# Kernel optimization log

Hardware: AMD Instinct MI355X
Metric: run time of the kernel (lower is better)

## Reference

```python
import jax, jax.numpy as jnp
import numpy as np

SWITCH_W = 30.0
TOL = 5
DECAY = 0.7
FP_PEN = 10.0
INV_PEN = 100.0
CLASS_W = jnp.array([1.0, 1.0, SWITCH_W, SWITCH_W], dtype=jnp.float32)


def setup_inputs() -> dict:
    key = jax.random.key(0)
    k1, k2, k3 = jax.random.split(key, 3)
    B, S, C = 512, 8192, 4
    logits = jax.random.normal(k1, (B, S, C), dtype=jnp.float32)
    labels = jax.random.randint(k2, (B, S), 0, 4, dtype=jnp.int32)
    # sprinkle ignore_index (-100) positions like real padded sequences
    drop = jax.random.uniform(k3, (B, S)) < 0.05
    labels = jnp.where(drop, jnp.int32(-100), labels)
    return {"logits": logits, "labels": labels}


def _mode_multiplier(labels, preds):
    """Sequential state machine over time; carry = (pred_mode, true_mode) per batch row."""
    B, S = labels.shape

    def step(carry, xs):
        pm, tm = carry
        lab, pred = xs  # [B] each
        valid = lab != -100
        # invalid transition penalty on predicted switches
        bad = ((pred == 2) & (pm == 0)) | ((pred == 3) & (pm == 1))
        pen = jnp.where(valid & bad, INV_PEN, 1.0)
        new_pm = jnp.where(valid, jnp.where((pred == 0) | (pred == 2), 0, 1), pm)
        # reward correct mode switches (true label agrees with pred switch)
        good = ((lab == 2) & (tm == 1) & (pred == 2)) | ((lab == 3) & (tm == 0) & (pred == 3))
        bonus = jnp.where(valid & good, 0.1, 1.0)
        new_tm = jnp.where(valid & ((lab == 0) | (lab == 2)), 0,
                           jnp.where(valid & ((lab == 1) | (lab == 3)), 1, tm))
        return (new_pm, new_tm), pen * bonus

    init = (jnp.zeros((B,), jnp.int32), jnp.zeros((B,), jnp.int32))
    _, mult = jax.lax.scan(step, init, (labels.T, preds.T))
    return mult.T  # [B, S]


def _nearest_dist(mask):
    """For each position, distance to nearest True in the same row; BIG if none."""
    B, S = mask.shape
    BIG = jnp.int32(S + TOL + 2)

    def f(c, m):
        c = jnp.where(m, jnp.int32(0), jnp.minimum(c + 1, BIG))
        return c, c

    init = jnp.full((B,), BIG, jnp.int32)
    _, fwd = jax.lax.scan(f, init, mask.T)
    _, bwd = jax.lax.scan(f, init, mask[:, ::-1].T)
    return jnp.minimum(fwd.T, bwd.T[:, ::-1])


def _loss(logits, labels):
    preds = jnp.argmax(logits, axis=-1).astype(jnp.int32)
    valid = labels != -100
    labs = jnp.where(valid, labels, 0)
    logp = jax.nn.log_softmax(logits, axis=-1)
    ce = -jnp.take_along_axis(logp, labs[..., None], axis=-1)[..., 0] * CLASS_W[labs]

    mult = _mode_multiplier(labels, preds)
    for c in (2, 3):
        true_m = labels == c
        pred_m = preds == c
        d_true = _nearest_dist(true_m)
        d_pred = _nearest_dist(pred_m)
        has_true = true_m.any(axis=1, keepdims=True)
        has_pred = pred_m.any(axis=1, keepdims=True)
        # multipliers at predicted-switch positions
        mp = jnp.where(
            pred_m,
            jnp.where(
                has_true,
                jnp.where(d_true == 0, 0.1,
                          jnp.where(d_true <= TOL, DECAY ** d_true.astype(jnp.float32), FP_PEN)),
                FP_PEN * 2.0),
            1.0)
        # multipliers at true-switch positions
        mt = jnp.where(
            true_m,
            jnp.where(has_pred, jnp.where(d_pred > TOL, 2.0, 1.0), 3.0),
            1.0)
        mult = mult * mp * mt

    vf = valid.astype(ce.dtype)
    total = (ce * mult * vf).sum()
    return total / jnp.maximum(vf.sum(), 1.0)


def reference(logits, labels):
    return _loss(logits, labels)
```

## Files before the change

kernel.cpp:

```cpp
#include <hip/hip_runtime.h>
#include <math.h>

#define BROWS 512
#define SLEN  8192
#define NT    1024
#define CHUNK (SLEN / NT)
#define NWRD  (SLEN / 32)
#define MWRD  (NWRD + 2)
#define CEPAD (SLEN + SLEN/8)

__device__ __forceinline__ int win_dist(const unsigned int* __restrict__ M, int t) {
    int sI = t + 27;
    int w  = sI >> 5;
    int off = sI & 31;
    unsigned long long val =
        ((unsigned long long)M[w] | ((unsigned long long)M[w + 1] << 32)) >> off;
    unsigned int win = (unsigned int)val & 0x7FFu;
    if (win & 32u) return 0;
    unsigned int dn = win & 31u;
    unsigned int up = (win >> 6) & 31u;
    int d = 99;
    if (dn) d = 5 - (31 - __clz((int)dn));
    if (up) { int du = __ffs((int)up); if (du < d) d = du; }
    return d;
}

__device__ __forceinline__ float decay_pow(int d) {
    return (d == 1) ? 0.7f : (d == 2) ? 0.49f : (d == 3) ? 0.343f
         : (d == 4) ? 0.2401f : 0.16807f;
}

__global__ __launch_bounds__(NT, 8) void row_loss_kernel(
    const float* __restrict__ logits, const int* __restrict__ labels,
    double* __restrict__ psum, unsigned int* __restrict__ pcnt)
{
    __shared__ float         s_ce[CEPAD];
    __shared__ unsigned char s_pk[SLEN];
    __shared__ unsigned int  s_m[4][MWRD];
    __shared__ unsigned int  s_wave[16];
    __shared__ unsigned int  s_wavex[16];
    __shared__ unsigned int  s_flags;
    __shared__ double        s_red[16];
    __shared__ int           s_redc[16];

    const int row  = blockIdx.x;
    const int tid  = threadIdx.x;
    const int lane = tid & 63;
    const int wid  = tid >> 6;

    for (int i = tid; i < 4 * MWRD; i += NT) ((unsigned int*)s_m)[i] = 0u;
    if (tid == 0) s_flags = 0u;

    const float4* lg4 = (const float4*)(logits + (size_t)row * SLEN * 4);
    const int*    lb  = labels + (size_t)row * SLEN;

    #pragma unroll
    for (int k = 0; k < CHUNK; ++k) {
        int t = k * NT + tid;
        float4 v = lg4[t];
        int lab = lb[t];
        int pred = 0; float best = v.x;
        if (v.y > best) { best = v.y; pred = 1; }
        if (v.z > best) { best = v.z; pred = 2; }
        if (v.w > best) { best = v.w; pred = 3; }
        bool valid = (lab != -100);
        int l = valid ? (lab & 3) : 0;
        float se = __expf(v.x - best) + __expf(v.y - best) +
                   __expf(v.z - best) + __expf(v.w - best);
        float lse = best + __logf(se);
        float xl = (l == 0) ? v.x : (l == 1) ? v.y : (l == 2) ? v.z : v.w;
        float wc = (l >= 2) ? 30.0f : 1.0f;
        s_ce[t + (t >> 3)] = valid ? (lse - xl) * wc : 0.0f;
        s_pk[t] = (unsigned char)(pred | (l << 2) | (valid ? 16 : 0));
    }
    __syncthreads();

    const int base = tid * CHUNK;
    unsigned int mt2 = 0, mp2 = 0, mt3 = 0, mp3 = 0;
    unsigned int summary = 0;
    #pragma unroll
    for (int i = 0; i < CHUNK; ++i) {
        unsigned int pk = s_pk[base + i];
        int pred = pk & 3, l = (pk >> 2) & 3;
        bool valid = (pk & 16) != 0;
        if (pred == 2) mp2 |= 1u << i;
        if (pred == 3) mp3 |= 1u << i;
        if (valid && l == 2) mt2 |= 1u << i;
        if (valid && l == 3) mt3 |= 1u << i;
        if (valid) summary = 4u | (unsigned)(pred & 1) | ((unsigned)(l & 1) << 1);
    }
    {
        int wi = 1 + (tid >> 2);
        int sh = (tid & 3) * 8;
        if (mt2) atomicOr(&s_m[0][wi], mt2 << sh);
        if (mp2) atomicOr(&s_m[1][wi], mp2 << sh);
        if (mt3) atomicOr(&s_m[2][wi], mt3 << sh);
        if (mp3) atomicOr(&s_m[3][wi], mp3 << sh);
    }
    {
        unsigned int fl = (mt2 ? 1u : 0u) | (mp2 ? 2u : 0u) |
                          (mt3 ? 4u : 0u) | (mp3 ? 8u : 0u);
        #pragma unroll
        for (int s = 32; s > 0; s >>= 1) fl |= __shfl_xor(fl, s);
        if (lane == 0 && fl) atomicOr(&s_flags, fl);
    }

    unsigned int inc = summary;
    #pragma unroll
    for (int st = 1; st < 64; st <<= 1) {
        unsigned int o = __shfl_up(inc, st);
        if (lane >= st && !(inc & 4u)) inc = o;
    }
    unsigned int exc = __shfl_up(inc, 1);
    if (lane == 0) exc = 0u;
    if (lane == 63) s_wave[wid] = inc;
    __syncthreads();
    if (wid == 0) {
        unsigned int wv = (lane < 16) ? s_wave[lane] : 0u;
        #pragma unroll
        for (int st = 1; st < 16; st <<= 1) {
            unsigned int o = __shfl_up(wv, st);
            if (lane >= st && !(wv & 4u)) wv = o;
        }
        unsigned int wex = __shfl_up(wv, 1);
        if (lane == 0) wex = 0u;
        if (lane < 16) s_wavex[lane] = wex;
    }
    __syncthreads();

    unsigned int pre = (exc & 4u) ? exc : s_wavex[wid];
    int pm = (int)(pre & 1u), tm = (int)((pre >> 1) & 1u);
    unsigned int flags = s_flags;
    const bool hasT2 = flags & 1u, hasP2 = flags & 2u;
    const bool hasT3 = flags & 4u, hasP3 = flags & 8u;

    float acc = 0.0f;
    int cnt = 0;
    #pragma unroll
    for (int i = 0; i < CHUNK; ++i) {
        int t = base + i;
        unsigned int pk = s_pk[t];
        int pred = pk & 3, l = (pk >> 2) & 3;
        bool valid = (pk & 16) != 0;
        float m = 1.0f;
        if (valid) {
            bool bad = (pred == 2 && pm == 0) || (pred == 3 && pm == 1);
            if (bad) m *= 100.0f;
            bool good = (l == 2 && tm == 1 && pred == 2) ||
                        (l == 3 && tm == 0 && pred == 3);
            if (good) m *= 0.1f;
            pm = pred & 1;
            tm = l & 1;
            cnt++;
        }
        if (pred == 2) {
            if (!hasT2) m *= 20.0f;
            else { int d = win_dist(s_m[0], t);
                   m *= (d == 0) ? 0.1f : (d <= 5) ? decay_pow(d) : 10.0f; }
        }
        if (valid && l == 2) {
            if (!hasP2) m *= 3.0f;
            else if (win_dist(s_m[1], t) > 5) m *= 2.0f;
        }
        if (pred == 3) {
            if (!hasT3) m *= 20.0f;
            else { int d = win_dist(s_m[2], t);
                   m *= (d == 0) ? 0.1f : (d <= 5) ? decay_pow(d) : 10.0f; }
        }
        if (valid && l == 3) {
            if (!hasP3) m *= 3.0f;
            else if (win_dist(s_m[3], t) > 5) m *= 2.0f;
        }
        acc += s_ce[tid * 9 + i] * m;
    }

    double dacc = (double)acc;
    #pragma unroll
    for (int o = 32; o > 0; o >>= 1) {
        dacc += __shfl_down(dacc, o);
        cnt  += __shfl_down(cnt, o);
    }
    if (lane == 0) { s_red[wid] = dacc; s_redc[wid] = cnt; }
    __syncthreads();
    if (tid == 0) {
        double tot = 0.0; unsigned int c = 0;
        #pragma unroll
        for (int i = 0; i < 16; ++i) { tot += s_red[i]; c += (unsigned int)s_redc[i]; }
        psum[row] = tot;
        pcnt[row] = c;
    }
}

__global__ __launch_bounds__(512) void finalize_kernel(
    const double* __restrict__ psum, const unsigned int* __restrict__ pcnt,
    float* __restrict__ out)
{
    __shared__ double       sd[8];
    __shared__ unsigned int sc[8];
    int tid = threadIdx.x, lane = tid & 63, wid = tid >> 6;
    double v = psum[tid];
    unsigned int c = pcnt[tid];
    #pragma unroll
    for (int o = 32; o > 0; o >>= 1) {
        v += __shfl_down(v, o);
        c += __shfl_down(c, o);
    }
    if (lane == 0) { sd[wid] = v; sc[wid] = c; }
    __syncthreads();
    if (tid == 0) {
        double t = 0.0; unsigned int cc = 0;
        #pragma unroll
        for (int i = 0; i < 8; ++i) { t += sd[i]; cc += sc[i]; }
        double d = (cc > 0u) ? (double)cc : 1.0;
        out[0] = (float)(t / d);
    }
}

extern "C" void kernel_launch(void* const* d_in, const int* in_sizes, int n_in,
                              void* d_out, int out_size, void* d_ws, size_t ws_size,
                              hipStream_t stream) {
    const float* logits = (const float*)d_in[0];
    const int*   labels = (const int*)d_in[1];
    float* out = (float*)d_out;
    double* psum = (double*)d_ws;
    unsigned int* pcnt = (unsigned int*)(psum + BROWS);

    row_loss_kernel<<<BROWS, NT, 0, stream>>>(logits, labels, psum, pcnt);
    finalize_kernel<<<1, 512, 0, stream>>>(psum, pcnt, out);
}
```

Before: 115.9 us.

## Batch global loads, vectorize LDS reads, replace mask atomics with shuffles

Loads four float4 logits and labels per thread before computing, which raises memory-level parallelism. Removes the padded CE layout in favour of contiguous float4 LDS reads per thread and reads packed bytes as one 64-bit word. Replaces the shared-memory atomicOr mask build with a quad shuffle-OR and plain stores, and zeroes only the halo words. Also merges the per-class distance branches and moves the valid count into the load loop. The contiguous s_ce writes with stride may add bank conflicts, and the extra in-flight loads raise register pressure.

Result: faster. 113.0 us (-2.4%).

```diff
diff --git a/kernel.cpp b/kernel.cpp
--- a/kernel.cpp
+++ b/kernel.cpp
@@ -7,7 +7,6 @@
 #define CHUNK (SLEN / NT)
 #define NWRD  (SLEN / 32)
 #define MWRD  (NWRD + 2)
-#define CEPAD (SLEN + SLEN/8)
 
 __device__ __forceinline__ int win_dist(const unsigned int* __restrict__ M, int t) {
     int sI = t + 27;
@@ -34,7 +33,7 @@
     const float* __restrict__ logits, const int* __restrict__ labels,
     double* __restrict__ psum, unsigned int* __restrict__ pcnt)
 {
-    __shared__ float         s_ce[CEPAD];
+    __shared__ float         s_ce[SLEN];
     __shared__ unsigned char s_pk[SLEN];
     __shared__ unsigned int  s_m[4][MWRD];
     __shared__ unsigned int  s_wave[16];
@@ -48,39 +47,51 @@
     const int lane = tid & 63;
     const int wid  = tid >> 6;
 
-    for (int i = tid; i < 4 * MWRD; i += NT) ((unsigned int*)s_m)[i] = 0u;
+    if (tid < 8) s_m[tid >> 1][(tid & 1) ? (MWRD - 1) : 0] = 0u;
     if (tid == 0) s_flags = 0u;
 
     const float4* lg4 = (const float4*)(logits + (size_t)row * SLEN * 4);
     const int*    lb  = labels + (size_t)row * SLEN;
 
-    #pragma unroll
-    for (int k = 0; k < CHUNK; ++k) {
-        int t = k * NT + tid;
-        float4 v = lg4[t];
-        int lab = lb[t];
-        int pred = 0; float best = v.x;
-        if (v.y > best) { best = v.y; pred = 1; }
-        if (v.z > best) { best = v.z; pred = 2; }
-        if (v.w > best) { best = v.w; pred = 3; }
-        bool valid = (lab != -100);
-        int l = valid ? (lab & 3) : 0;
-        float se = __expf(v.x - best) + __expf(v.y - best) +
-                   __expf(v.z - best) + __expf(v.w - best);
-        float lse = best + __logf(se);
-        float xl = (l == 0) ? v.x : (l == 1) ? v.y : (l == 2) ? v.z : v.w;
-        float wc = (l >= 2) ? 30.0f : 1.0f;
-        s_ce[t + (t >> 3)] = valid ? (lse - xl) * wc : 0.0f;
-        s_pk[t] = (unsigned char)(pred | (l << 2) | (valid ? 16 : 0));
+    int cnt = 0;
+    #pragma unroll
+    for (int kk = 0; kk < CHUNK; kk += 4) {
+        float4 v[4]; int la[4];
+        #pragma unroll
+        for (int j = 0; j < 4; ++j) {
+            int t = (kk + j) * NT + tid;
+            v[j]  = lg4[t];
+            la[j] = lb[t];
+        }
+        #pragma unroll
+        for (int j = 0; j < 4; ++j) {
+            int t = (kk + j) * NT + tid;
+            float4 q = v[j];
+            int lab  = la[j];
+            float m01 = fmaxf(q.x, q.y), m23 = fmaxf(q.z, q.w);
+            float best = fmaxf(m01, m23);
+            int pred = (best == q.x) ? 0 : (best == q.y) ? 1 : (best == q.z) ? 2 : 3;
+            bool valid = (lab != -100);
+            cnt += valid ? 1 : 0;
+            int l = valid ? (lab & 3) : 0;
+            float se = __expf(q.x - best) + __expf(q.y - best) +
+                       __expf(q.z - best) + __expf(q.w - best);
+            float lse = best + __logf(se);
+            float xl = (l == 0) ? q.x : (l == 1) ? q.y : (l == 2) ? q.z : q.w;
+            float wc = (l >= 2) ? 30.0f : 1.0f;
+            s_ce[t] = valid ? (lse - xl) * wc : 0.0f;
+            s_pk[t] = (unsigned char)(pred | (l << 2) | (valid ? 16 : 0));
+        }
     }
     __syncthreads();
 
     const int base = tid * CHUNK;
+    const unsigned long long pkw = *(const unsigned long long*)(s_pk + base);
     unsigned int mt2 = 0, mp2 = 0, mt3 = 0, mp3 = 0;
     unsigned int summary = 0;
     #pragma unroll
     for (int i = 0; i < CHUNK; ++i) {
-        unsigned int pk = s_pk[base + i];
+        unsigned int pk = (unsigned int)(pkw >> (8 * i)) & 31u;
         int pred = pk & 3, l = (pk >> 2) & 3;
         bool valid = (pk & 16) != 0;
         if (pred == 2) mp2 |= 1u << i;
@@ -90,12 +101,16 @@
         if (valid) summary = 4u | (unsigned)(pred & 1) | ((unsigned)(l & 1) << 1);
     }
     {
-        int wi = 1 + (tid >> 2);
         int sh = (tid & 3) * 8;
-        if (mt2) atomicOr(&s_m[0][wi], mt2 << sh);
-        if (mp2) atomicOr(&s_m[1][wi], mp2 << sh);
-        if (mt3) atomicOr(&s_m[2][wi], mt3 << sh);
-        if (mp3) atomicOr(&s_m[3][wi], mp3 << sh);
+        unsigned int w0 = mt2 << sh, w1 = mp2 << sh, w2 = mt3 << sh, w3 = mp3 << sh;
+        w0 |= __shfl_xor(w0, 1); w0 |= __shfl_xor(w0, 2);
+        w1 |= __shfl_xor(w1, 1); w1 |= __shfl_xor(w1, 2);
+        w2 |= __shfl_xor(w2, 1); w2 |= __shfl_xor(w2, 2);
+        w3 |= __shfl_xor(w3, 1); w3 |= __shfl_xor(w3, 2);
+        if ((tid & 3) == 0) {
+            int wi = 1 + (tid >> 2);
+            s_m[0][wi] = w0; s_m[1][wi] = w1; s_m[2][wi] = w2; s_m[3][wi] = w3;
+        }
     }
     {
         unsigned int fl = (mt2 ? 1u : 0u) | (mp2 ? 2u : 0u) |
@@ -130,16 +145,19 @@
 
     unsigned int pre = (exc & 4u) ? exc : s_wavex[wid];
     int pm = (int)(pre & 1u), tm = (int)((pre >> 1) & 1u);
-    unsigned int flags = s_flags;
+    const unsigned int flags = s_flags;
     const bool hasT2 = flags & 1u, hasP2 = flags & 2u;
     const bool hasT3 = flags & 4u, hasP3 = flags & 8u;
 
+    float4 c0 = *(const float4*)(s_ce + base);
+    float4 c1 = *(const float4*)(s_ce + base + 4);
+    float cearr[8] = {c0.x, c0.y, c0.z, c0.w, c1.x, c1.y, c1.z, c1.w};
+
     float acc = 0.0f;
-    int cnt = 0;
     #pragma unroll
     for (int i = 0; i < CHUNK; ++i) {
         int t = base + i;
-        unsigned int pk = s_pk[t];
+        unsigned int pk = (unsigned int)(pkw >> (8 * i)) & 31u;
         int pred = pk & 3, l = (pk >> 2) & 3;
         bool valid = (pk & 16) != 0;
         float m = 1.0f;
@@ -151,27 +169,21 @@
             if (good) m *= 0.1f;
             pm = pred & 1;
             tm = l & 1;
-            cnt++;
-        }
-        if (pred == 2) {
-            if (!hasT2) m *= 20.0f;
-            else { int d = win_dist(s_m[0], t);
-                   m *= (d == 0) ? 0.1f : (d <= 5) ? decay_pow(d) : 10.0f; }
-        }
-        if (valid && l == 2) {
-            if (!hasP2) m *= 3.0f;
-            else if (win_dist(s_m[1], t) > 5) m *= 2.0f;
-        }
-        if (pred == 3) {
-            if (!hasT3) m *= 20.0f;
-            else { int d = win_dist(s_m[2], t);
-                   m *= (d == 0) ? 0.1f : (d <= 5) ? decay_pow(d) : 10.0f; }
-        }
-        if (valid && l == 3) {
-            if (!hasP3) m *= 3.0f;
-            else if (win_dist(s_m[3], t) > 5) m *= 2.0f;
-        }
-        acc += s_ce[tid * 9 + i] * m;
+        }
+        if (pred >= 2) {
+            bool has = (pred == 2) ? hasT2 : hasT3;
+            if (!has) m *= 20.0f;
+            else {
+                int d = win_dist(s_m[(pred - 2) << 1], t);
+                m *= (d == 0) ? 0.1f : (d <= 5) ? decay_pow(d) : 10.0f;
+            }
+        }
+        if (valid && l >= 2) {
+            bool has = (l == 2) ? hasP2 : hasP3;
+            if (!has) m *= 3.0f;
+            else if (win_dist(s_m[1 + ((l - 2) << 1)], t) > 5) m *= 2.0f;
+        }
+        acc += cearr[i] * m;
     }
 
     double dacc = (double)acc;
```
